# Kernel tuning notes

Measured on AMD Instinct MI355X. Metric: run time of the kernel, lower is better.

The kernel has to match this reference:

```python
import jax, jax.numpy as jnp
import numpy as np

N_RAYS = 65536
N_SAMPLES = 96


def setup_inputs() -> dict:
    key = jax.random.key(0)
    k1, k2, k3 = jax.random.split(key, 3)
    rgb = jax.random.uniform(k1, (N_RAYS, N_SAMPLES, 3), dtype=jnp.float32)
    # SDF values near the surface, small magnitude
    sdf = jax.random.normal(k2, (N_RAYS, N_SAMPLES), dtype=jnp.float32) * 0.1
    # monotonically increasing sample depths along each ray
    z_vals = jnp.sort(
        jax.random.uniform(k3, (N_RAYS, N_SAMPLES), dtype=jnp.float32,
                           minval=0.1, maxval=5.0), axis=-1)
    return {"rgb": rgb, "sdf": sdf, "z_vals": z_vals, "beta": 10}


def reference(rgb, sdf, z_vals, beta):
    # sdf2alpha: alpha = 1 - exp(-beta * sigmoid(-sdf * beta))
    alpha = 1.0 - jnp.exp(-beta * jax.nn.sigmoid(-sdf * beta))  # [N, S]
    # exclusive cumprod of (1 - alpha + 1e-10): transmittance
    trans = jnp.cumprod(
        jnp.concatenate([jnp.ones_like(alpha[:, :1]), 1.0 - alpha + 1e-10],
                        axis=-1), axis=-1)[:, :-1]  # [N, S]
    weights = alpha * trans  # [N, S]
    rendered_rgb = jnp.sum(weights[..., None] * rgb, axis=-2)  # [N, 3]
    rendered_depth = jnp.sum(weights * z_vals, axis=-1)  # [N]
    return (rendered_depth, rendered_rgb, sdf, z_vals)
```

## Files before the change

### kernel.cpp

```cpp
#include <hip/hip_runtime.h>
#include <hip/hip_bf16.h>


#define SDFR_N_SAMPLES 96

__global__ __launch_bounds__(256) void sdf_render_kernel(
    const float*  __restrict__ rgb,
    const float*  __restrict__ sdf,
    const float*  __restrict__ zv,
    const int*    __restrict__ beta_p,
    float* __restrict__ out_depth,
    float* __restrict__ out_rgb,
    float* __restrict__ out_sdf,
    float* __restrict__ out_z,
    int n_rays)
{
    int bi = *beta_p;
    float beta;
    if (bi > 1000000 || bi < -1000000) {
        union { int i; float f; } c; c.i = bi; beta = c.f;
    } else {
        beta = (float)bi;
    }

    const int lane = threadIdx.x & 63;
    const int half = lane >> 5;
    const int l    = lane & 31;
    const int wave = threadIdx.x >> 6;
    const int ray  = (blockIdx.x * 4 + wave) * 2 + half;
    if (ray >= n_rays) return;
    const int base = ray * SDFR_N_SAMPLES;

    float carry = 1.0f;
    float depth = 0.0f, r0 = 0.0f, r1 = 0.0f, r2 = 0.0f;

    #pragma unroll
    for (int k = 0; k < 3; ++k) {
        const int idx = base + 32 * k + l;
        const float sdf_f = sdf[idx];
        const float z_f   = zv[idx];
        out_sdf[idx] = sdf_f;
        out_z[idx]   = z_f;

        const float x   = -sdf_f * beta;
        const float sig = 1.0f / (1.0f + __expf(-x));
        const float e   = __expf(-beta * sig);
        const float alpha = 1.0f - e;
        const float t     = e + 1e-10f;

        float scan = t;
        #pragma unroll
        for (int d = 1; d < 32; d <<= 1) {
            float v = __shfl_up(scan, d, 32);
            if (l >= d) scan *= v;
        }
        const float excl = __shfl_up(scan, 1, 32);
        const float P = carry * ((l == 0) ? 1.0f : excl);
        const float w = alpha * P;

        depth += w * z_f;
        const float3 c = *(const float3*)(rgb + (size_t)idx * 3);
        r0 += w * c.x;
        r1 += w * c.y;
        r2 += w * c.z;

        carry *= __shfl(scan, 31, 32);
    }

    #pragma unroll
    for (int d = 16; d >= 1; d >>= 1) {
        depth += __shfl_xor(depth, d, 32);
        r0    += __shfl_xor(r0, d, 32);
        r1    += __shfl_xor(r1, d, 32);
        r2    += __shfl_xor(r2, d, 32);
    }

    if (l == 0) {
        out_depth[ray]       = depth;
        out_rgb[ray * 3 + 0] = r0;
        out_rgb[ray * 3 + 1] = r1;
        out_rgb[ray * 3 + 2] = r2;
    }
}

extern "C" void kernel_launch(void* const* d_in, const int* in_sizes, int n_in,
                              void* d_out, int out_size, void* d_ws, size_t ws_size,
                              hipStream_t stream) {
    (void)n_in; (void)d_ws; (void)ws_size; (void)out_size;

    const float* rgb    = (const float*)d_in[0];
    const float* sdf    = (const float*)d_in[1];
    const float* zv     = (const float*)d_in[2];
    const int*   beta_p = (const int*)d_in[3];

    const int n_rays = in_sizes[1] / SDFR_N_SAMPLES;

    float* out_depth = (float*)d_out;
    float* out_rgb   = out_depth + n_rays;
    float* out_sdf   = out_rgb   + (size_t)n_rays * 3;
    float* out_z     = out_sdf   + (size_t)n_rays * SDFR_N_SAMPLES;

    const int rays_per_block = 8;
    const int grid = (n_rays + rays_per_block - 1) / rays_per_block;
    sdf_render_kernel<<<grid, 256, 0, stream>>>(
        rgb, sdf, zv, beta_p, out_depth, out_rgb, out_sdf, out_z, n_rays);
}
```

Baseline: 169.8 us.

## Process three contiguous samples per lane with a single warp scan

Each lane now owns three consecutive samples of the ray instead of three strided ones. Their local transmittance product is combined in one 32-lane shuffle scan instead of three, and the sigmoid uses a hardware reciprocal. This cuts shuffle and scan latency. In exchange, the loads and stores become stride-3 per lane, which may hurt coalescing compared with the previous unit-stride access, and products are taken in a different order.

Measured after the change: 169.8 us. Within noise of the previous version (+0.0%).

```diff
diff --git a/kernel.cpp b/kernel.cpp
--- a/kernel.cpp
+++ b/kernel.cpp
@@ -29,43 +29,52 @@
     const int wave = threadIdx.x >> 6;
     const int ray  = (blockIdx.x * 4 + wave) * 2 + half;
     if (ray >= n_rays) return;
-    const int base = ray * SDFR_N_SAMPLES;
 
-    float carry = 1.0f;
-    float depth = 0.0f, r0 = 0.0f, r1 = 0.0f, r2 = 0.0f;
+    const int base = ray * SDFR_N_SAMPLES + 3 * l;
 
+    const float s0 = sdf[base + 0];
+    const float s1 = sdf[base + 1];
+    const float s2 = sdf[base + 2];
+    const float z0 = zv[base + 0];
+    const float z1 = zv[base + 1];
+    const float z2 = zv[base + 2];
+    const float* rp = rgb + (size_t)base * 3;
+    float c[9];
     #pragma unroll
-    for (int k = 0; k < 3; ++k) {
-        const int idx = base + 32 * k + l;
-        const float sdf_f = sdf[idx];
-        const float z_f   = zv[idx];
-        out_sdf[idx] = sdf_f;
-        out_z[idx]   = z_f;
+    for (int i = 0; i < 9; ++i) c[i] = rp[i];
 
-        const float x   = -sdf_f * beta;
-        const float sig = 1.0f / (1.0f + __expf(-x));
-        const float e   = __expf(-beta * sig);
-        const float alpha = 1.0f - e;
-        const float t     = e + 1e-10f;
+    out_sdf[base + 0] = s0;
+    out_sdf[base + 1] = s1;
+    out_sdf[base + 2] = s2;
+    out_z[base + 0]   = z0;
+    out_z[base + 1]   = z1;
+    out_z[base + 2]   = z2;
 
-        float scan = t;
-        #pragma unroll
-        for (int d = 1; d < 32; d <<= 1) {
-            float v = __shfl_up(scan, d, 32);
-            if (l >= d) scan *= v;
-        }
-        const float excl = __shfl_up(scan, 1, 32);
-        const float P = carry * ((l == 0) ? 1.0f : excl);
-        const float w = alpha * P;
+    const float e0 = __expf(-beta * __builtin_amdgcn_rcpf(1.0f + __expf(s0 * beta)));
+    const float e1 = __expf(-beta * __builtin_amdgcn_rcpf(1.0f + __expf(s1 * beta)));
+    const float e2 = __expf(-beta * __builtin_amdgcn_rcpf(1.0f + __expf(s2 * beta)));
+    const float a0 = 1.0f - e0, t0 = e0 + 1e-10f;
+    const float a1 = 1.0f - e1, t1 = e1 + 1e-10f;
+    const float a2 = 1.0f - e2, t2 = e2 + 1e-10f;
 
-        depth += w * z_f;
-        const float3 c = *(const float3*)(rgb + (size_t)idx * 3);
-        r0 += w * c.x;
-        r1 += w * c.y;
-        r2 += w * c.z;
+    const float m = t0 * t1 * t2;
+    float scan = m;
+    #pragma unroll
+    for (int d = 1; d < 32; d <<= 1) {
+        float v = __shfl_up(scan, d, 32);
+        if (l >= d) scan *= v;
+    }
+    float E = __shfl_up(scan, 1, 32);
+    if (l == 0) E = 1.0f;
 
-        carry *= __shfl(scan, 31, 32);
-    }
+    const float w0 = a0 * E;
+    const float w1 = a1 * E * t0;
+    const float w2 = a2 * E * t0 * t1;
+
+    float depth = w0 * z0 + w1 * z1 + w2 * z2;
+    float r0 = w0 * c[0] + w1 * c[3] + w2 * c[6];
+    float r1 = w0 * c[1] + w1 * c[4] + w2 * c[7];
+    float r2 = w0 * c[2] + w1 * c[5] + w2 * c[8];
 
     #pragma unroll
     for (int d = 16; d >= 1; d >>= 1) {
```

## Assign eight lanes per ray with float4 loads and a serial-then-shuffle scan

Applied to the files above, without the earlier changes.

Each ray is now handled by 8 lanes instead of 32. Each lane loads 12 consecutive samples of sdf and z plus their rgb values as float4 vectors, and copies sdf and z to the outputs with float4 stores. The transmittance cumprod becomes a per-lane serial product, followed by a 3-step shuffle scan across 8 lanes, which replaces the 5-step 32-lane scan that ran three times per ray. The aim is fewer, wider memory transactions and fewer shuffles, at the cost of more registers per thread and a strided per-lane access pattern within each wave.

Result: slower. 185.8 us (+9.5%).

```diff
diff --git a/kernel.cpp b/kernel.cpp
--- a/kernel.cpp
+++ b/kernel.cpp
@@ -2,80 +2,97 @@
 #include <hip/hip_bf16.h>
 
 
-#define SDFR_N_SAMPLES 96
+#define SDFR_NS 96
 
-__global__ __launch_bounds__(256) void sdf_render_kernel(
-    const float*  __restrict__ rgb,
-    const float*  __restrict__ sdf,
-    const float*  __restrict__ zv,
+__global__ __launch_bounds__(256, 4) void sdf_render_kernel(
+    const float4* __restrict__ sdf4,
+    const float4* __restrict__ z4,
+    const float4* __restrict__ rgb4,
     const int*    __restrict__ beta_p,
-    float* __restrict__ out_depth,
-    float* __restrict__ out_rgb,
-    float* __restrict__ out_sdf,
-    float* __restrict__ out_z,
+    float*  __restrict__ out_depth,
+    float*  __restrict__ out_rgb,
+    float4* __restrict__ out_sdf4,
+    float4* __restrict__ out_z4,
     int n_rays)
 {
+    const int t    = threadIdx.x;
+    const int wave = t >> 6;
+    const int lane = t & 63;
+    const int seg  = lane >> 3;
+    const int sl   = lane & 7;
+
+    const int ray = blockIdx.x * 32 + wave * 8 + seg;
+    if (ray >= n_rays) return;
+
+    const int b4  = ray * (SDFR_NS / 4) + sl * 3;
+    const int rb4 = ray * (SDFR_NS * 3 / 4) + sl * 9;
+
+    float4 s[3], z[3], c[9];
+    #pragma unroll
+    for (int i = 0; i < 3; ++i) s[i] = sdf4[b4 + i];
+    #pragma unroll
+    for (int i = 0; i < 3; ++i) z[i] = z4[b4 + i];
+    #pragma unroll
+    for (int i = 0; i < 9; ++i) c[i] = rgb4[rb4 + i];
+
     int bi = *beta_p;
     float beta;
     if (bi > 1000000 || bi < -1000000) {
-        union { int i; float f; } c; c.i = bi; beta = c.f;
+        union { int i; float f; } u; u.i = bi; beta = u.f;
     } else {
         beta = (float)bi;
     }
 
-    const int lane = threadIdx.x & 63;
-    const int half = lane >> 5;
-    const int l    = lane & 31;
-    const int wave = threadIdx.x >> 6;
-    const int ray  = (blockIdx.x * 4 + wave) * 2 + half;
-    if (ray >= n_rays) return;
-    const int base = ray * SDFR_N_SAMPLES;
+    #pragma unroll
+    for (int i = 0; i < 3; ++i) out_sdf4[b4 + i] = s[i];
+    #pragma unroll
+    for (int i = 0; i < 3; ++i) out_z4[b4 + i] = z[i];
 
-    float carry = 1.0f;
+    const float* sf = (const float*)s;
+    const float* zf = (const float*)z;
+    const float* cf = (const float*)c;
+    float tv[12], av[12];
+    #pragma unroll
+    for (int j = 0; j < 12; ++j) {
+        const float e = __expf(-beta * __builtin_amdgcn_rcpf(1.0f + __expf(sf[j] * beta)));
+        av[j] = 1.0f - e;
+        tv[j] = e + 1e-10f;
+    }
+
+    float m = 1.0f;
+    #pragma unroll
+    for (int j = 0; j < 12; ++j) m *= tv[j];
+
+    float scan = m;
+    #pragma unroll
+    for (int d = 1; d < 8; d <<= 1) {
+        float v = __shfl_up(scan, d, 8);
+        if (sl >= d) scan *= v;
+    }
+    float E = __shfl_up(scan, 1, 8);
+    if (sl == 0) E = 1.0f;
+
     float depth = 0.0f, r0 = 0.0f, r1 = 0.0f, r2 = 0.0f;
-
+    float p = E;
     #pragma unroll
-    for (int k = 0; k < 3; ++k) {
-        const int idx = base + 32 * k + l;
-        const float sdf_f = sdf[idx];
-        const float z_f   = zv[idx];
-        out_sdf[idx] = sdf_f;
-        out_z[idx]   = z_f;
-
-        const float x   = -sdf_f * beta;
-        const float sig = 1.0f / (1.0f + __expf(-x));
-        const float e   = __expf(-beta * sig);
-        const float alpha = 1.0f - e;
-        const float t     = e + 1e-10f;
-
-        float scan = t;
-        #pragma unroll
-        for (int d = 1; d < 32; d <<= 1) {
-            float v = __shfl_up(scan, d, 32);
-            if (l >= d) scan *= v;
-        }
-        const float excl = __shfl_up(scan, 1, 32);
-        const float P = carry * ((l == 0) ? 1.0f : excl);
-        const float w = alpha * P;
-
-        depth += w * z_f;
-        const float3 c = *(const float3*)(rgb + (size_t)idx * 3);
-        r0 += w * c.x;
-        r1 += w * c.y;
-        r2 += w * c.z;
-
-        carry *= __shfl(scan, 31, 32);
+    for (int j = 0; j < 12; ++j) {
+        const float w = av[j] * p;
+        depth += w * zf[j];
+        r0 += w * cf[3 * j + 0];
+        r1 += w * cf[3 * j + 1];
+        r2 += w * cf[3 * j + 2];
+        p *= tv[j];
     }
 
     #pragma unroll
-    for (int d = 16; d >= 1; d >>= 1) {
-        depth += __shfl_xor(depth, d, 32);
-        r0    += __shfl_xor(r0, d, 32);
-        r1    += __shfl_xor(r1, d, 32);
-        r2    += __shfl_xor(r2, d, 32);
+    for (int d = 4; d >= 1; d >>= 1) {
+        depth += __shfl_xor(depth, d, 8);
+        r0    += __shfl_xor(r0, d, 8);
+        r1    += __shfl_xor(r1, d, 8);
+        r2    += __shfl_xor(r2, d, 8);
     }
 
-    if (l == 0) {
+    if (sl == 0) {
         out_depth[ray]       = depth;
         out_rgb[ray * 3 + 0] = r0;
         out_rgb[ray * 3 + 1] = r1;
@@ -88,20 +105,20 @@
                               hipStream_t stream) {
     (void)n_in; (void)d_ws; (void)ws_size; (void)out_size;
 
-    const float* rgb    = (const float*)d_in[0];
-    const float* sdf    = (const float*)d_in[1];
-    const float* zv     = (const float*)d_in[2];
-    const int*   beta_p = (const int*)d_in[3];
+    const float4* rgb4   = (const float4*)d_in[0];
+    const float4* sdf4   = (const float4*)d_in[1];
+    const float4* z4     = (const float4*)d_in[2];
+    const int*    beta_p = (const int*)d_in[3];
 
-    const int n_rays = in_sizes[1] / SDFR_N_SAMPLES;
+    const int n_rays = in_sizes[1] / SDFR_NS;
 
     float* out_depth = (float*)d_out;
     float* out_rgb   = out_depth + n_rays;
     float* out_sdf   = out_rgb   + (size_t)n_rays * 3;
-    float* out_z     = out_sdf   + (size_t)n_rays * SDFR_N_SAMPLES;
+    float* out_z     = out_sdf   + (size_t)n_rays * SDFR_NS;
 
-    const int rays_per_block = 8;
-    const int grid = (n_rays + rays_per_block - 1) / rays_per_block;
+    const int grid = (n_rays + 31) / 32;
     sdf_render_kernel<<<grid, 256, 0, stream>>>(
-        rgb, sdf, zv, beta_p, out_depth, out_rgb, out_sdf, out_z, n_rays);
+        sdf4, z4, rgb4, beta_p, out_depth, out_rgb,
+        (float4*)out_sdf, (float4*)out_z, n_rays);
 }
```
